# Performance work log

Hardware: AMD Instinct MI355X
Metric: run time of the kernel (lower is better)

The kernel has to match this reference:

```python
import jax, jax.numpy as jnp
import numpy as np

N, E, F_IN, C, OUT = 50000, 800000, 256, 64, 2
NEG_SLOPE = 0.2  # PyG GATv2Conv default


def setup_inputs() -> dict:
    key = jax.random.key(0)
    ks = jax.random.split(key, 12)
    s = 0.05
    return {
        "x": jax.random.normal(ks[0], (N, F_IN), jnp.float32),
        "edge_index": jax.random.randint(ks[1], (2, E), 0, N, jnp.int64),
        "edge_attr": jax.random.uniform(ks[2], (E, 1), jnp.float32),
        # GATv2Conv params (heads=1): lin_l, lin_r (with bias), lin_edge (no bias), att, conv bias
        "Wl": jax.random.normal(ks[3], (C, F_IN), jnp.float32) * s,
        "bl": jax.random.normal(ks[4], (C,), jnp.float32) * s,
        "Wr": jax.random.normal(ks[5], (C, F_IN), jnp.float32) * s,
        "br": jax.random.normal(ks[6], (C,), jnp.float32) * s,
        "We": jax.random.normal(ks[7], (C, 1), jnp.float32) * s,
        "att": jax.random.normal(ks[8], (C,), jnp.float32) * s,
        "b_conv": jax.random.normal(ks[9], (C,), jnp.float32) * s,
        # final linear head
        "W_head": jax.random.normal(ks[10], (OUT, C), jnp.float32) * s,
        "b_head": jax.random.normal(ks[11], (OUT,), jnp.float32) * s,
    }


def reference(x, edge_index, edge_attr, Wl, bl, Wr, br, We, att, b_conv, W_head, b_head):
    n = x.shape[0]
    xl = x @ Wl.T + bl  # [N, C] source transform (values)
    xr = x @ Wr.T + br  # [N, C] destination transform
    src, dst = edge_index[0], edge_index[1]

    # add self loops; self-loop edge_attr = mean of incoming edge attrs (fill_value='mean')
    cnt = jax.ops.segment_sum(jnp.ones(src.shape, x.dtype), dst, num_segments=n)
    loop_attr = jax.ops.segment_sum(edge_attr, dst, num_segments=n) / jnp.clip(cnt, 1.0)[:, None]
    ar = jnp.arange(n, dtype=src.dtype)
    src2 = jnp.concatenate([src, ar])
    dst2 = jnp.concatenate([dst, ar])
    ea2 = jnp.concatenate([edge_attr, loop_attr], axis=0)

    # GATv2 attention: score = att . leaky_relu(xl[src] + xr[dst] + We @ ea)
    m = xl[src2] + xr[dst2] + ea2 @ We.T  # [E+N, C]
    e = jnp.sum(jax.nn.leaky_relu(m, NEG_SLOPE) * att, axis=-1)  # [E+N]

    # per-destination softmax (every node has a self loop -> no empty segments)
    emax = jax.lax.stop_gradient(jax.ops.segment_max(e, dst2, num_segments=n))
    ee = jnp.exp(e - emax[dst2])
    denom = jax.ops.segment_sum(ee, dst2, num_segments=n)
    alpha = ee / denom[dst2]  # [E+N]

    out = jax.ops.segment_sum(alpha[:, None] * xl[src2], dst2, num_segments=n) + b_conv  # [N, C]

    h = jax.nn.relu(out)                      # dropout is identity in eval mode
    pooled = jnp.mean(h, axis=0, keepdims=True)  # MeanAggregation over all nodes -> [1, C]
    logits = pooled @ W_head.T + b_head          # [1, 2]
    return jax.nn.softmax(logits, axis=-1)
```

## Files before the change

### kernel.cpp

```cpp
#include <hip/hip_runtime.h>

constexpr int NN   = 50000;
constexpr int EE   = 800000;
constexpr float NEG_SLOPE = 0.2f;
constexpr int NREG  = 8;
constexpr int RCAP  = 16;
constexpr int SLOTS = NREG * RCAP;
constexpr int PSROWS = NN / 4;

typedef __attribute__((ext_vector_type(4))) float f32x4;
typedef __attribute__((ext_vector_type(8))) short bf16x8;

constexpr size_t OFF_XLB   = 0;
constexpr size_t OFF_XRB   = OFF_XLB  + (size_t)NN * 64 * 2;
constexpr size_t OFF_PSUM  = OFF_XRB  + (size_t)NN * 64 * 2;
constexpr size_t OFF_FILL8 = OFF_PSUM + (size_t)PSROWS * 64 * 4;
constexpr size_t OFF_POOL  = OFF_FILL8+ (size_t)NREG * NN * 4;
constexpr size_t OFF_CSRP  = OFF_POOL + 256;
constexpr size_t ZERO_BYTES = (size_t)NREG * NN * 4 + 256;

__device__ __forceinline__ unsigned short f2bf(float f) {
    unsigned u = __float_as_uint(f);
    unsigned r = (u + 0x7FFFu + ((u >> 16) & 1u)) >> 16;
    return (unsigned short)r;
}
__device__ __forceinline__ float bf2f(unsigned s) {
    return __uint_as_float(s << 16);
}

constexpr int GEMM_BLOCKS = 391;
constexpr int SCAT_BLOCKS = 512;
constexpr int GEMM_WAVES  = GEMM_BLOCKS * 8;
constexpr int NSTRIP      = NN / 16;

__global__ __launch_bounds__(512, 2)
void fused_gemm_scatter(const float* __restrict__ x,
                        const float* __restrict__ Wl, const float* __restrict__ bl,
                        const float* __restrict__ Wr, const float* __restrict__ br,
                        unsigned short* __restrict__ xlb, unsigned short* __restrict__ xrb,
                        const int* __restrict__ ei, const float* __restrict__ ea,
                        int* __restrict__ fill8, unsigned* __restrict__ csrp) {
    if (blockIdx.x >= GEMM_BLOCKS) {
        const int b   = blockIdx.x - GEMM_BLOCKS;
        const int reg = blockIdx.x & 7;
        int* fr = fill8 + reg * NN;
        for (int e = b * 512 + threadIdx.x; e < EE; e += SCAT_BLOCKS * 512) {
            int src = ei[e];
            int dst = ei[EE + e];
            unsigned pk = (unsigned)src | ((unsigned)f2bf(ea[e]) << 16);
            int k = atomicAdd(&fr[dst], 1);
            if (k < RCAP) csrp[(size_t)dst * SLOTS + reg * RCAP + k] = pk;
        }
        return;
    }

    extern __shared__ bf16x8 Wf[];
    const int tid  = threadIdx.x;
    const int lane = tid & 63;
    const int w    = tid >> 6;

    for (int idx = tid; idx < 4096; idx += 512) {
        int cb = idx >> 9;
        int ks = (idx >> 6) & 7;
        int l  = idx & 63;
        int r16 = l & 15, g = l >> 4;
        const float* wsrc = (cb < 4) ? (Wl + (size_t)(16 * cb + r16) * 256)
                                     : (Wr + (size_t)(16 * (cb - 4) + r16) * 256);
        int k0 = 32 * ks + 8 * g;
        float4 w0 = *reinterpret_cast<const float4*>(wsrc + k0);
        float4 w1 = *reinterpret_cast<const float4*>(wsrc + k0 + 4);
        bf16x8 pk;
        pk[0] = (short)f2bf(w0.x); pk[1] = (short)f2bf(w0.y);
        pk[2] = (short)f2bf(w0.z); pk[3] = (short)f2bf(w0.w);
        pk[4] = (short)f2bf(w1.x); pk[5] = (short)f2bf(w1.y);
        pk[6] = (short)f2bf(w1.z); pk[7] = (short)f2bf(w1.w);
        Wf[idx] = pk;
    }

    const int col15 = lane & 15;
    const int g4    = lane >> 4;
    float bias[8];
    #pragma unroll
    for (int cb = 0; cb < 8; ++cb)
        bias[cb] = (cb < 4) ? bl[16 * cb + col15] : br[16 * (cb - 4) + col15];
    __syncthreads();

    const int gw = blockIdx.x * 8 + w;
    for (int strip = gw; strip < NSTRIP; strip += GEMM_WAVES) {
        const int r0 = strip * 16;
        const float* xrow = x + (size_t)(r0 + col15) * 256 + 8 * g4;

        f32x4 acc[8];
        #pragma unroll
        for (int cb = 0; cb < 8; ++cb) acc[cb] = (f32x4){0.f, 0.f, 0.f, 0.f};

        #pragma unroll
        for (int ks = 0; ks < 8; ++ks) {
            float4 a0 = *reinterpret_cast<const float4*>(xrow + 32 * ks);
            float4 a1 = *reinterpret_cast<const float4*>(xrow + 32 * ks + 4);
            bf16x8 af;
            af[0] = (short)f2bf(a0.x); af[1] = (short)f2bf(a0.y);
            af[2] = (short)f2bf(a0.z); af[3] = (short)f2bf(a0.w);
            af[4] = (short)f2bf(a1.x); af[5] = (short)f2bf(a1.y);
            af[6] = (short)f2bf(a1.z); af[7] = (short)f2bf(a1.w);
            #pragma unroll
            for (int cb = 0; cb < 8; ++cb) {
                bf16x8 bfg = Wf[(cb * 8 + ks) * 64 + lane];
                acc[cb] = __builtin_amdgcn_mfma_f32_16x16x32_bf16(af, bfg, acc[cb], 0, 0, 0);
            }
        }

        #pragma unroll
        for (int cb = 0; cb < 8; ++cb) {
            unsigned short* dst = (cb < 4) ? xlb : xrb;
            int c0 = (cb & 3) * 16 + col15;
            #pragma unroll
            for (int r = 0; r < 4; ++r) {
                int row = r0 + 4 * g4 + r;
                dst[(size_t)row * 64 + c0] = f2bf(acc[cb][r] + bias[cb]);
            }
        }
    }
}

__global__ __launch_bounds__(256)
void attn_kernel(const unsigned short* __restrict__ xlb, const unsigned short* __restrict__ xrb,
                 const uint2* __restrict__ csrp2, const int* __restrict__ fill8,
                 const float* __restrict__ We, const float* __restrict__ att,
                 const float* __restrict__ bconv, float* __restrict__ psum) {
    __shared__ unsigned ebuf[4][SLOTS];
    __shared__ float sred[256];
    const int wid = threadIdx.x >> 6;
    const int c   = threadIdx.x & 63;
    const int v   = blockIdx.x * 4 + wid;

    const float wec = We[c], attc = att[c];
    const float xrc = bf2f(xrb[(size_t)v * 64 + c]);
    const float xlc = bf2f(xlb[(size_t)v * 64 + c]);

    uint2 ep   = csrp2[(size_t)v * (SLOTS / 2) + c];
    int   myr  = c >> 3;
    int   mycnt = fill8[myr * NN + v];
    int   mycc  = min(mycnt, RCAP);
    int prefC = 0, degT = 0, degC = 0;
    #pragma unroll
    for (int r = 0; r < 8; ++r) {
        int cr = __shfl(mycnt, r * 8);
        int cc = min(cr, RCAP);
        degT += cr; degC += cc;
        if (r < myr) prefC += cc;
    }
    int k0 = (2 * c) & 15;
    if (k0     < mycc) ebuf[wid][prefC + k0]     = ep.x;
    if (k0 + 1 < mycc) ebuf[wid][prefC + k0 + 1] = ep.y;
    __syncthreads();

    const unsigned* eb = ebuf[wid];
    float dA = 0.f, dB = 0.f, aA = 0.f, aB = 0.f, asum = 0.f;

    const int nch = degC >> 3;
    uint4 EA, EB, FA, FB;
    float x0, x1, x2, x3, x4, x5, x6, x7;
    float y0, y1, y2, y3, y4, y5, y6, y7;

    if (nch > 0) {
        EA = *reinterpret_cast<const uint4*>(&eb[0]);
        EB = *reinterpret_cast<const uint4*>(&eb[4]);
        x0 = bf2f(xlb[(size_t)(EA.x & 0xFFFFu) * 64 + c]);
        x1 = bf2f(xlb[(size_t)(EA.y & 0xFFFFu) * 64 + c]);
        x2 = bf2f(xlb[(size_t)(EA.z & 0xFFFFu) * 64 + c]);
        x3 = bf2f(xlb[(size_t)(EA.w & 0xFFFFu) * 64 + c]);
        x4 = bf2f(xlb[(size_t)(EB.x & 0xFFFFu) * 64 + c]);
        x5 = bf2f(xlb[(size_t)(EB.y & 0xFFFFu) * 64 + c]);
        x6 = bf2f(xlb[(size_t)(EB.z & 0xFFFFu) * 64 + c]);
        x7 = bf2f(xlb[(size_t)(EB.w & 0xFFFFu) * 64 + c]);
    }
    for (int ch = 0; ch < nch; ++ch) {
        if (ch + 1 < nch) {
            FA = *reinterpret_cast<const uint4*>(&eb[(ch + 1) * 8]);
            FB = *reinterpret_cast<const uint4*>(&eb[(ch + 1) * 8 + 4]);
            y0 = bf2f(xlb[(size_t)(FA.x & 0xFFFFu) * 64 + c]);
            y1 = bf2f(xlb[(size_t)(FA.y & 0xFFFFu) * 64 + c]);
            y2 = bf2f(xlb[(size_t)(FA.z & 0xFFFFu) * 64 + c]);
            y3 = bf2f(xlb[(size_t)(FA.w & 0xFFFFu) * 64 + c]);
            y4 = bf2f(xlb[(size_t)(FB.x & 0xFFFFu) * 64 + c]);
            y5 = bf2f(xlb[(size_t)(FB.y & 0xFFFFu) * 64 + c]);
            y6 = bf2f(xlb[(size_t)(FB.z & 0xFFFFu) * 64 + c]);
            y7 = bf2f(xlb[(size_t)(FB.w & 0xFFFFu) * 64 + c]);
        }
        float at0 = bf2f(EA.x >> 16), at1 = bf2f(EA.y >> 16);
        float at2 = bf2f(EA.z >> 16), at3 = bf2f(EA.w >> 16);
        float at4 = bf2f(EB.x >> 16), at5 = bf2f(EB.y >> 16);
        float at6 = bf2f(EB.z >> 16), at7 = bf2f(EB.w >> 16);
        asum += (at0 + at1 + at2 + at3) + (at4 + at5 + at6 + at7);

        float m, s0, s1, s2, s3, s4, s5, s6, s7;
        m = fmaf(wec, at0, x0 + xrc); s0 = fmaf(NEG_SLOPE, fminf(m, 0.f), fmaxf(m, 0.f)) * attc;
        m = fmaf(wec, at1, x1 + xrc); s1 = fmaf(NEG_SLOPE, fminf(m, 0.f), fmaxf(m, 0.f)) * attc;
        m = fmaf(wec, at2, x2 + xrc); s2 = fmaf(NEG_SLOPE, fminf(m, 0.f), fmaxf(m, 0.f)) * attc;
        m = fmaf(wec, at3, x3 + xrc); s3 = fmaf(NEG_SLOPE, fminf(m, 0.f), fmaxf(m, 0.f)) * attc;
        m = fmaf(wec, at4, x4 + xrc); s4 = fmaf(NEG_SLOPE, fminf(m, 0.f), fmaxf(m, 0.f)) * attc;
        m = fmaf(wec, at5, x5 + xrc); s5 = fmaf(NEG_SLOPE, fminf(m, 0.f), fmaxf(m, 0.f)) * attc;
        m = fmaf(wec, at6, x6 + xrc); s6 = fmaf(NEG_SLOPE, fminf(m, 0.f), fmaxf(m, 0.f)) * attc;
        m = fmaf(wec, at7, x7 + xrc); s7 = fmaf(NEG_SLOPE, fminf(m, 0.f), fmaxf(m, 0.f)) * attc;

        #pragma unroll
        for (int d = 1; d < 64; d <<= 1) {
            s0 += __shfl_xor(s0, d); s1 += __shfl_xor(s1, d);
            s2 += __shfl_xor(s2, d); s3 += __shfl_xor(s3, d);
            s4 += __shfl_xor(s4, d); s5 += __shfl_xor(s5, d);
            s6 += __shfl_xor(s6, d); s7 += __shfl_xor(s7, d);
        }

        float p;
        p = __expf(s0); dA += p; aA = fmaf(p, x0, aA);
        p = __expf(s1); dB += p; aB = fmaf(p, x1, aB);
        p = __expf(s2); dA += p; aA = fmaf(p, x2, aA);
        p = __expf(s3); dB += p; aB = fmaf(p, x3, aB);
        p = __expf(s4); dA += p; aA = fmaf(p, x4, aA);
        p = __expf(s5); dB += p; aB = fmaf(p, x5, aB);
        p = __expf(s6); dA += p; aA = fmaf(p, x6, aA);
        p = __expf(s7); dB += p; aB = fmaf(p, x7, aB);

        EA = FA; EB = FB;
        x0 = y0; x1 = y1; x2 = y2; x3 = y3;
        x4 = y4; x5 = y5; x6 = y6; x7 = y7;
    }
    for (int j = nch * 8; j < degC; ++j) {
        unsigned e = eb[j];
        float at = bf2f(e >> 16);
        float xx = bf2f(xlb[(size_t)(e & 0xFFFFu) * 64 + c]);
        asum += at;
        float m = fmaf(wec, at, xx + xrc);
        float s = fmaf(NEG_SLOPE, fminf(m, 0.f), fmaxf(m, 0.f)) * attc;
        #pragma unroll
        for (int d = 1; d < 64; d <<= 1) s += __shfl_xor(s, d);
        float p = __expf(s);
        dA += p; aA = fmaf(p, xx, aA);
    }

    {
        float lattr = asum / fmaxf((float)degT, 1.0f);
        float m = fmaf(wec, lattr, xlc + xrc);
        float s = fmaf(NEG_SLOPE, fminf(m, 0.f), fmaxf(m, 0.f)) * attc;
        #pragma unroll
        for (int d = 1; d < 64; d <<= 1) s += __shfl_xor(s, d);
        float p = __expf(s);
        dA += p; aA = fmaf(p, xlc, aA);
    }

    float outv = fmaxf((aA + aB) / (dA + dB) + bconv[c], 0.0f);
    sred[threadIdx.x] = outv;
    __syncthreads();
    if (threadIdx.x < 64) {
        psum[(size_t)blockIdx.x * 64 + c] =
            sred[c] + sred[64 + c] + sred[128 + c] + sred[192 + c];
    }
}

__global__ void pool_kernel(const float* __restrict__ psum, float* __restrict__ pool) {
    __shared__ float s[256];
    const int c = threadIdx.x & 63, g = threadIdx.x >> 6;
    float acc = 0.f;
    for (int r = blockIdx.x * 4 + g; r < PSROWS; r += gridDim.x * 4)
        acc += psum[(size_t)r * 64 + c];
    s[threadIdx.x] = acc;
    __syncthreads();
    if (threadIdx.x < 64) {
        float tot = s[c] + s[64 + c] + s[128 + c] + s[192 + c];
        atomicAdd(&pool[c], tot);
    }
}

__global__ void head_kernel(const float* __restrict__ pool, const float* __restrict__ Wh,
                            const float* __restrict__ bh, float* __restrict__ out) {
    const int c = threadIdx.x;
    float p  = pool[c] * (1.0f / (float)NN);
    float a0 = p * Wh[c];
    float a1 = p * Wh[64 + c];
    #pragma unroll
    for (int d = 1; d < 64; d <<= 1) { a0 += __shfl_xor(a0, d); a1 += __shfl_xor(a1, d); }
    if (c == 0) {
        float l0 = a0 + bh[0], l1 = a1 + bh[1];
        float mx = fmaxf(l0, l1);
        float e0 = __expf(l0 - mx), e1 = __expf(l1 - mx);
        float inv = 1.0f / (e0 + e1);
        out[0] = e0 * inv;
        out[1] = e1 * inv;
    }
}

extern "C" void kernel_launch(void* const* d_in, const int* in_sizes, int n_in,
                              void* d_out, int out_size, void* d_ws, size_t ws_size,
                              hipStream_t stream) {
    const float* x    = (const float*)d_in[0];
    const int*   ei   = (const int*)  d_in[1];
    const float* ea   = (const float*)d_in[2];
    const float* Wl   = (const float*)d_in[3];
    const float* bl   = (const float*)d_in[4];
    const float* Wr   = (const float*)d_in[5];
    const float* br   = (const float*)d_in[6];
    const float* We   = (const float*)d_in[7];
    const float* att  = (const float*)d_in[8];
    const float* bcv  = (const float*)d_in[9];
    const float* Wh   = (const float*)d_in[10];
    const float* bh   = (const float*)d_in[11];
    float* out = (float*)d_out;

    char* ws = (char*)d_ws;
    unsigned short* xlb = (unsigned short*)(ws + OFF_XLB);
    unsigned short* xrb = (unsigned short*)(ws + OFF_XRB);
    float*    psum  = (float*)   (ws + OFF_PSUM);
    int*      fill8 = (int*)     (ws + OFF_FILL8);
    float*    pool  = (float*)   (ws + OFF_POOL);
    unsigned* csrp  = (unsigned*)(ws + OFF_CSRP);

    hipMemsetAsync(ws + OFF_FILL8, 0, ZERO_BYTES, stream);

    fused_gemm_scatter<<<GEMM_BLOCKS + SCAT_BLOCKS, 512, 4096 * sizeof(bf16x8), stream>>>(
        x, Wl, bl, Wr, br, xlb, xrb, ei, ea, fill8, csrp);

    attn_kernel<<<NN / 4, 256, 0, stream>>>(xlb, xrb, (const uint2*)csrp, fill8,
                                            We, att, bcv, psum);

    pool_kernel<<<64, 256, 0, stream>>>(psum, pool);
    head_kernel<<<1, 64, 0, stream>>>(pool, Wh, bh, out);
}
```

Before: 234.7 us.

## Process 8 edges per wave with 8 lanes per edge using vector loads

Restructures attention aggregation so each wave handles 8 edges at once, with each lane owning 8 channels loaded as a single 16-byte bf16 vector. The 6-step full-wave reduction per edge shrinks to a 3-step reduction within 8 lanes, and the accumulators are combined across edge slots with butterfly shuffles at the end. This cuts shuffle count and gather instructions per edge. In exchange, the prefetch of the next chunk is removed, a padded tail is handled by masking, and each lane now keeps more registers.

After: 212.9 us. 1.1x faster.

```diff
diff --git a/kernel.cpp b/kernel.cpp
--- a/kernel.cpp
+++ b/kernel.cpp
@@ -10,6 +10,7 @@
 
 typedef __attribute__((ext_vector_type(4))) float f32x4;
 typedef __attribute__((ext_vector_type(8))) short bf16x8;
+typedef __attribute__((ext_vector_type(8))) unsigned short u16x8;
 
 constexpr size_t OFF_XLB   = 0;
 constexpr size_t OFF_XRB   = OFF_XLB  + (size_t)NN * 64 * 2;
@@ -129,17 +130,16 @@
                  const float* __restrict__ We, const float* __restrict__ att,
                  const float* __restrict__ bconv, float* __restrict__ psum) {
     __shared__ unsigned ebuf[4][SLOTS];
-    __shared__ float sred[256];
+    __shared__ float sred[4][64];
     const int wid = threadIdx.x >> 6;
     const int c   = threadIdx.x & 63;
     const int v   = blockIdx.x * 4 + wid;
-
-    const float wec = We[c], attc = att[c];
-    const float xrc = bf2f(xrb[(size_t)v * 64 + c]);
-    const float xlc = bf2f(xlb[(size_t)v * 64 + c]);
-
-    uint2 ep   = csrp2[(size_t)v * (SLOTS / 2) + c];
-    int   myr  = c >> 3;
+    const int g   = c & 7;
+    const int c0  = g * 8;
+    const int es  = c >> 3;
+
+    uint2 ep    = csrp2[(size_t)v * (SLOTS / 2) + c];
+    int   myr   = c >> 3;
     int   mycnt = fill8[myr * NN + v];
     int   mycc  = min(mycnt, RCAP);
     int prefC = 0, degT = 0, degC = 0;
@@ -153,108 +153,88 @@
     int k0 = (2 * c) & 15;
     if (k0     < mycc) ebuf[wid][prefC + k0]     = ep.x;
     if (k0 + 1 < mycc) ebuf[wid][prefC + k0 + 1] = ep.y;
+    if (c < 8 && degC + c < SLOTS) ebuf[wid][degC + c] = 0;
     __syncthreads();
 
+    float wv[8], av[8], xrv[8];
+    {
+        u16x8 xr8 = *reinterpret_cast<const u16x8*>(&xrb[(size_t)v * 64 + c0]);
+        float4 w0 = *reinterpret_cast<const float4*>(&We[c0]);
+        float4 w1 = *reinterpret_cast<const float4*>(&We[c0 + 4]);
+        float4 a0 = *reinterpret_cast<const float4*>(&att[c0]);
+        float4 a1 = *reinterpret_cast<const float4*>(&att[c0 + 4]);
+        wv[0] = w0.x; wv[1] = w0.y; wv[2] = w0.z; wv[3] = w0.w;
+        wv[4] = w1.x; wv[5] = w1.y; wv[6] = w1.z; wv[7] = w1.w;
+        av[0] = a0.x; av[1] = a0.y; av[2] = a0.z; av[3] = a0.w;
+        av[4] = a1.x; av[5] = a1.y; av[6] = a1.z; av[7] = a1.w;
+        #pragma unroll
+        for (int j = 0; j < 8; ++j) xrv[j] = bf2f(xr8[j]);
+    }
+
     const unsigned* eb = ebuf[wid];
-    float dA = 0.f, dB = 0.f, aA = 0.f, aB = 0.f, asum = 0.f;
-
-    const int nch = degC >> 3;
-    uint4 EA, EB, FA, FB;
-    float x0, x1, x2, x3, x4, x5, x6, x7;
-    float y0, y1, y2, y3, y4, y5, y6, y7;
-
-    if (nch > 0) {
-        EA = *reinterpret_cast<const uint4*>(&eb[0]);
-        EB = *reinterpret_cast<const uint4*>(&eb[4]);
-        x0 = bf2f(xlb[(size_t)(EA.x & 0xFFFFu) * 64 + c]);
-        x1 = bf2f(xlb[(size_t)(EA.y & 0xFFFFu) * 64 + c]);
-        x2 = bf2f(xlb[(size_t)(EA.z & 0xFFFFu) * 64 + c]);
-        x3 = bf2f(xlb[(size_t)(EA.w & 0xFFFFu) * 64 + c]);
-        x4 = bf2f(xlb[(size_t)(EB.x & 0xFFFFu) * 64 + c]);
-        x5 = bf2f(xlb[(size_t)(EB.y & 0xFFFFu) * 64 + c]);
-        x6 = bf2f(xlb[(size_t)(EB.z & 0xFFFFu) * 64 + c]);
-        x7 = bf2f(xlb[(size_t)(EB.w & 0xFFFFu) * 64 + c]);
-    }
+    float acc[8] = {0.f, 0.f, 0.f, 0.f, 0.f, 0.f, 0.f, 0.f};
+    float dsum = 0.f, asum = 0.f;
+    const int nch = (degC + 7) >> 3;
+
     for (int ch = 0; ch < nch; ++ch) {
-        if (ch + 1 < nch) {
-            FA = *reinterpret_cast<const uint4*>(&eb[(ch + 1) * 8]);
-            FB = *reinterpret_cast<const uint4*>(&eb[(ch + 1) * 8 + 4]);
-            y0 = bf2f(xlb[(size_t)(FA.x & 0xFFFFu) * 64 + c]);
-            y1 = bf2f(xlb[(size_t)(FA.y & 0xFFFFu) * 64 + c]);
-            y2 = bf2f(xlb[(size_t)(FA.z & 0xFFFFu) * 64 + c]);
-            y3 = bf2f(xlb[(size_t)(FA.w & 0xFFFFu) * 64 + c]);
-            y4 = bf2f(xlb[(size_t)(FB.x & 0xFFFFu) * 64 + c]);
-            y5 = bf2f(xlb[(size_t)(FB.y & 0xFFFFu) * 64 + c]);
-            y6 = bf2f(xlb[(size_t)(FB.z & 0xFFFFu) * 64 + c]);
-            y7 = bf2f(xlb[(size_t)(FB.w & 0xFFFFu) * 64 + c]);
-        }
-        float at0 = bf2f(EA.x >> 16), at1 = bf2f(EA.y >> 16);
-        float at2 = bf2f(EA.z >> 16), at3 = bf2f(EA.w >> 16);
-        float at4 = bf2f(EB.x >> 16), at5 = bf2f(EB.y >> 16);
-        float at6 = bf2f(EB.z >> 16), at7 = bf2f(EB.w >> 16);
-        asum += (at0 + at1 + at2 + at3) + (at4 + at5 + at6 + at7);
-
-        float m, s0, s1, s2, s3, s4, s5, s6, s7;
-        m = fmaf(wec, at0, x0 + xrc); s0 = fmaf(NEG_SLOPE, fminf(m, 0.f), fmaxf(m, 0.f)) * attc;
-        m = fmaf(wec, at1, x1 + xrc); s1 = fmaf(NEG_SLOPE, fminf(m, 0.f), fmaxf(m, 0.f)) * attc;
-        m = fmaf(wec, at2, x2 + xrc); s2 = fmaf(NEG_SLOPE, fminf(m, 0.f), fmaxf(m, 0.f)) * attc;
-        m = fmaf(wec, at3, x3 + xrc); s3 = fmaf(NEG_SLOPE, fminf(m, 0.f), fmaxf(m, 0.f)) * attc;
-        m = fmaf(wec, at4, x4 + xrc); s4 = fmaf(NEG_SLOPE, fminf(m, 0.f), fmaxf(m, 0.f)) * attc;
-        m = fmaf(wec, at5, x5 + xrc); s5 = fmaf(NEG_SLOPE, fminf(m, 0.f), fmaxf(m, 0.f)) * attc;
-        m = fmaf(wec, at6, x6 + xrc); s6 = fmaf(NEG_SLOPE, fminf(m, 0.f), fmaxf(m, 0.f)) * attc;
-        m = fmaf(wec, at7, x7 + xrc); s7 = fmaf(NEG_SLOPE, fminf(m, 0.f), fmaxf(m, 0.f)) * attc;
-
-        #pragma unroll
-        for (int d = 1; d < 64; d <<= 1) {
-            s0 += __shfl_xor(s0, d); s1 += __shfl_xor(s1, d);
-            s2 += __shfl_xor(s2, d); s3 += __shfl_xor(s3, d);
-            s4 += __shfl_xor(s4, d); s5 += __shfl_xor(s5, d);
-            s6 += __shfl_xor(s6, d); s7 += __shfl_xor(s7, d);
-        }
-
-        float p;
-        p = __expf(s0); dA += p; aA = fmaf(p, x0, aA);
-        p = __expf(s1); dB += p; aB = fmaf(p, x1, aB);
-        p = __expf(s2); dA += p; aA = fmaf(p, x2, aA);
-        p = __expf(s3); dB += p; aB = fmaf(p, x3, aB);
-        p = __expf(s4); dA += p; aA = fmaf(p, x4, aA);
-        p = __expf(s5); dB += p; aB = fmaf(p, x5, aB);
-        p = __expf(s6); dA += p; aA = fmaf(p, x6, aA);
-        p = __expf(s7); dB += p; aB = fmaf(p, x7, aB);
-
-        EA = FA; EB = FB;
-        x0 = y0; x1 = y1; x2 = y2; x3 = y3;
-        x4 = y4; x5 = y5; x6 = y6; x7 = y7;
-    }
-    for (int j = nch * 8; j < degC; ++j) {
-        unsigned e = eb[j];
-        float at = bf2f(e >> 16);
-        float xx = bf2f(xlb[(size_t)(e & 0xFFFFu) * 64 + c]);
-        asum += at;
-        float m = fmaf(wec, at, xx + xrc);
-        float s = fmaf(NEG_SLOPE, fminf(m, 0.f), fmaxf(m, 0.f)) * attc;
-        #pragma unroll
-        for (int d = 1; d < 64; d <<= 1) s += __shfl_xor(s, d);
+        const int eidx = ch * 8 + es;
+        unsigned e = eb[eidx];
+        const bool valid = eidx < degC;
+        float attr = bf2f(e >> 16);
+        u16x8 xv = *reinterpret_cast<const u16x8*>(&xlb[(size_t)(e & 0xFFFFu) * 64 + c0]);
+        float xf[8];
+        float s = 0.f;
+        #pragma unroll
+        for (int j = 0; j < 8; ++j) {
+            xf[j] = bf2f(xv[j]);
+            float m = fmaf(wv[j], attr, xf[j] + xrv[j]);
+            s = fmaf(fmaf(NEG_SLOPE, fminf(m, 0.f), fmaxf(m, 0.f)), av[j], s);
+        }
+        s += __shfl_xor(s, 1); s += __shfl_xor(s, 2); s += __shfl_xor(s, 4);
+        float p = valid ? __expf(s) : 0.f;
+        dsum += p;
+        asum += valid ? attr : 0.f;
+        #pragma unroll
+        for (int j = 0; j < 8; ++j) acc[j] = fmaf(p, xf[j], acc[j]);
+    }
+
+    #pragma unroll
+    for (int d = 8; d < 64; d <<= 1) {
+        dsum += __shfl_xor(dsum, d);
+        asum += __shfl_xor(asum, d);
+        #pragma unroll
+        for (int j = 0; j < 8; ++j) acc[j] += __shfl_xor(acc[j], d);
+    }
+
+    float xlf[8];
+    {
+        u16x8 xl8 = *reinterpret_cast<const u16x8*>(&xlb[(size_t)v * 64 + c0]);
+        float lattr = asum / fmaxf((float)degT, 1.0f);
+        float s = 0.f;
+        #pragma unroll
+        for (int j = 0; j < 8; ++j) {
+            xlf[j] = bf2f(xl8[j]);
+            float m = fmaf(wv[j], lattr, xlf[j] + xrv[j]);
+            s = fmaf(fmaf(NEG_SLOPE, fminf(m, 0.f), fmaxf(m, 0.f)), av[j], s);
+        }
+        s += __shfl_xor(s, 1); s += __shfl_xor(s, 2); s += __shfl_xor(s, 4);
         float p = __expf(s);
-        dA += p; aA = fmaf(p, xx, aA);
-    }
-
-    {
-        float lattr = asum / fmaxf((float)degT, 1.0f);
-        float m = fmaf(wec, lattr, xlc + xrc);
-        float s = fmaf(NEG_SLOPE, fminf(m, 0.f), fmaxf(m, 0.f)) * attc;
-        #pragma unroll
-        for (int d = 1; d < 64; d <<= 1) s += __shfl_xor(s, d);
-        float p = __expf(s);
-        dA += p; aA = fmaf(p, xlc, aA);
-    }
-
-    float outv = fmaxf((aA + aB) / (dA + dB) + bconv[c], 0.0f);
-    sred[threadIdx.x] = outv;
+        dsum += p;
+        #pragma unroll
+        for (int j = 0; j < 8; ++j) acc[j] = fmaf(p, xlf[j], acc[j]);
+    }
+
+    if (es == 0) {
+        float inv = 1.0f / dsum;
+        #pragma unroll
+        for (int j = 0; j < 8; ++j)
+            sred[wid][c0 + j] = fmaxf(fmaf(acc[j], inv, bconv[c0 + j]), 0.0f);
+    }
     __syncthreads();
     if (threadIdx.x < 64) {
-        psum[(size_t)blockIdx.x * 64 + c] =
-            sred[c] + sred[64 + c] + sred[128 + c] + sred[192 + c];
+        psum[(size_t)blockIdx.x * 64 + threadIdx.x] =
+            sred[0][threadIdx.x] + sred[1][threadIdx.x] +
+            sred[2][threadIdx.x] + sred[3][threadIdx.x];
     }
 }
 
```
